# Optimization experiments

Hardware: AMD Instinct MI355X
Metric: run time of the kernel (lower is better)

The kernel has to match this reference:

```python
import jax, jax.numpy as jnp
import numpy as np
import math

D_MODEL, N_LEVELS, N_HEADS, N_POINTS = 256, 4, 8, 4
D_HEAD = D_MODEL // N_HEADS
SPATIAL = np.array([[128, 128], [64, 64], [32, 32], [16, 16]], dtype=np.int32)  # (H_l, W_l)
LEN_IN = int((SPATIAL[:, 0] * SPATIAL[:, 1]).sum())  # 21760
N_BATCH, LEN_Q = 8, 1000


def _offset_bias():
    # torch _reset_parameters grid_init
    thetas = np.arange(N_HEADS, dtype=np.float32) * (2.0 * math.pi / N_HEADS)
    grid = np.stack([np.cos(thetas), np.sin(thetas)], -1)
    grid = grid / np.abs(grid).max(-1, keepdims=True)
    grid = np.tile(grid.reshape(N_HEADS, 1, 1, 2), (1, N_LEVELS, N_POINTS, 1))
    for i in range(N_POINTS):
        grid[:, :, i, :] *= i + 1
    return jnp.asarray(grid.reshape(-1), dtype=jnp.float32)


def setup_inputs() -> dict:
    key = jax.random.key(0)
    ks = jax.random.split(key, 8)
    s = 1.0 / math.sqrt(D_MODEL)
    return {
        "query": jax.random.normal(ks[0], (N_BATCH, LEN_Q, D_MODEL), jnp.float32),
        "reference_points": jax.random.uniform(ks[1], (N_BATCH, LEN_Q, N_LEVELS, 2), jnp.float32),
        "input_flatten": jax.random.normal(ks[2], (N_BATCH, LEN_IN, D_MODEL), jnp.float32),
        "input_spatial_shapes": jnp.asarray(SPATIAL),
        "input_level_start_index": jnp.asarray(np.concatenate([[0], np.cumsum(SPATIAL[:, 0] * SPATIAL[:, 1])[:-1]]).astype(np.int32)),
        # params (W stored as (in, out); y = x @ W + b)
        "W_off": jax.random.normal(ks[3], (D_MODEL, N_HEADS * N_LEVELS * N_POINTS * 2), jnp.float32) * 0.01,
        "b_off": _offset_bias(),
        "W_attn": jax.random.normal(ks[4], (D_MODEL, N_HEADS * N_LEVELS * N_POINTS), jnp.float32) * 0.02,
        "b_attn": jnp.zeros((N_HEADS * N_LEVELS * N_POINTS,), jnp.float32),
        "W_val": jax.random.normal(ks[5], (D_MODEL, D_MODEL), jnp.float32) * s,
        "b_val": jnp.zeros((D_MODEL,), jnp.float32),
        "W_out": jax.random.normal(ks[6], (D_MODEL, D_MODEL), jnp.float32) * s,
        "b_out": jnp.zeros((D_MODEL,), jnp.float32),
    }


def _bilinear_sample(v, x, y, H, W):
    # v: (N, nH, H*W, dH); x, y: (N, nH, Lq, nP) in pixel coords (grid_sample align_corners=False, zeros padding)
    Nb, nH, Lq, nP = x.shape
    x0 = jnp.floor(x); y0 = jnp.floor(y)
    wx1 = x - x0; wy1 = y - y0
    x0i = x0.astype(jnp.int32); y0i = y0.astype(jnp.int32)
    out = jnp.zeros((Nb, nH, Lq, nP, v.shape[-1]), v.dtype)
    for dy, wy in ((0, 1.0 - wy1), (1, wy1)):
        for dx, wx in ((0, 1.0 - wx1), (1, wx1)):
            ix = x0i + dx; iy = y0i + dy
            valid = (ix >= 0) & (ix < W) & (iy >= 0) & (iy < H)
            idx = (jnp.clip(iy, 0, H - 1) * W + jnp.clip(ix, 0, W - 1)).reshape(Nb, nH, Lq * nP, 1)
            g = jnp.take_along_axis(v, idx, axis=2).reshape(Nb, nH, Lq, nP, -1)
            out = out + g * (wy * wx * valid.astype(v.dtype))[..., None]
    return out


def reference(query, reference_points, input_flatten, input_spatial_shapes, input_level_start_index,
              W_off, b_off, W_attn, b_attn, W_val, b_val, W_out, b_out):
    shapes = np.asarray(input_spatial_shapes)          # static metadata
    starts = np.asarray(input_level_start_index)
    Nb, Lq, _ = query.shape

    value = input_flatten @ W_val + b_val              # (N, Lin, C)
    value = value.reshape(Nb, -1, N_HEADS, D_HEAD).transpose(0, 2, 1, 3)  # (N, nH, Lin, dH)

    offsets = (query @ W_off + b_off).reshape(Nb, Lq, N_HEADS, N_LEVELS, N_POINTS, 2)
    attn = jax.nn.softmax((query @ W_attn + b_attn).reshape(Nb, Lq, N_HEADS, N_LEVELS * N_POINTS), axis=-1)
    attn = attn.reshape(Nb, Lq, N_HEADS, N_LEVELS, N_POINTS)

    # normalizer is (W_l, H_l) per level; locations in [0,1]
    normalizer = jnp.asarray(np.stack([shapes[:, 1], shapes[:, 0]], -1), jnp.float32)
    loc = reference_points[:, :, None, :, None, :] + offsets / normalizer[None, None, None, :, None, :]

    out = jnp.zeros((Nb, N_HEADS, Lq, D_HEAD), value.dtype)
    for l in range(N_LEVELS):
        H, W = int(shapes[l, 0]), int(shapes[l, 1])
        s = int(starts[l])
        v_l = value[:, :, s:s + H * W]                             # (N, nH, HW, dH)
        loc_l = loc[:, :, :, l].transpose(0, 2, 1, 3, 4)           # (N, nH, Lq, nP, 2)
        x = loc_l[..., 0] * W - 0.5
        y = loc_l[..., 1] * H - 0.5
        sampled = _bilinear_sample(v_l, x, y, H, W)                # (N, nH, Lq, nP, dH)
        a_l = attn[:, :, :, l].transpose(0, 2, 1, 3)               # (N, nH, Lq, nP)
        out = out + jnp.einsum('nhqpd,nhqp->nhqd', sampled, a_l)

    out = out.transpose(0, 2, 1, 3).reshape(Nb, Lq, D_MODEL)
    return out @ W_out + b_out
```

## Files before the change

kernel.cpp:

```cpp
#include <hip/hip_runtime.h>
#include <hip/hip_bf16.h>

#define D_MODEL 256
#define N_HEADS 8
#define D_HEAD 32
#define N_LEVELS 4
#define N_POINTS 4
#define LEN_IN 21760
#define N_BATCH 8
#define LEN_Q 1000

typedef __attribute__((ext_vector_type(8))) short short8;
typedef __attribute__((ext_vector_type(4))) float f32x4;
typedef __attribute__((ext_vector_type(4))) unsigned int u32x4;

typedef const __attribute__((address_space(1))) void* gp1;
typedef __attribute__((address_space(3))) void* lp3;

__device__ __forceinline__ unsigned short f2bf(float f) {
    unsigned int u = __float_as_uint(f);
    u += 0x7FFFu + ((u >> 16) & 1u);
    return (unsigned short)(u >> 16);
}
__device__ __forceinline__ float bf2f(unsigned short s) {
    return __uint_as_float(((unsigned int)s) << 16);
}

__global__ __launch_bounds__(256) void prep_kernel(
    const float* __restrict__ Wv, const float* __restrict__ Wo,
    const float* __restrict__ Wa, const float* __restrict__ Wu,
    const float* __restrict__ boff, const float* __restrict__ battn,
    unsigned short* __restrict__ WtVp, unsigned short* __restrict__ WtC,
    unsigned short* __restrict__ WtO, float* __restrict__ bcat)
{
    int idx = blockIdx.x * 256 + threadIdx.x;
    if (idx < 65536) {
        int j = idx & 7, lane = (idx >> 3) & 63, nf = (idx >> 9) & 15, ks = idx >> 13;
        int col = nf * 16 + (lane & 15);
        int k = ks * 32 + (lane >> 4) * 8 + j;
        WtVp[idx] = f2bf(Wv[k * 256 + col]);
    } else if (idx < 65536 + 98304) {
        int j = idx - 65536;
        int n = j >> 8, k = j & 255;
        float s = (n < 256) ? Wo[k * 256 + n] : Wa[k * 128 + (n - 256)];
        WtC[j] = f2bf(s);
    } else if (idx < 65536 + 98304 + 65536) {
        int j = idx - (65536 + 98304);
        int n = j >> 8, k = j & 255;
        WtO[j] = f2bf(Wu[k * 256 + n]);
    } else if (idx < 65536 + 98304 + 65536 + 384) {
        int j = idx - (65536 + 98304 + 65536);
        bcat[j] = (j < 256) ? boff[j] : battn[j - 256];
    }
}

__global__ __launch_bounds__(256) void gemm_value(
    const float* __restrict__ A,
    const unsigned short* __restrict__ Bp,
    const float* __restrict__ bias,
    unsigned short* __restrict__ C)
{
    __shared__ float lds[2][2048];

    const int tid = threadIdx.x;
    const int wave = tid >> 6, lane = tid & 63;
    const int lhi = lane >> 4, llo = lane & 15;
    const int mBase = blockIdx.x * 64;

    const int soff = tid * 16;
    const int r0 = soff >> 7, cb0 = soff & 127;
    const size_t g0 = (size_t)r0 * 1024 + (size_t)(cb0 ^ ((r0 & 7) << 4));
    const size_t g1 = g0 + (size_t)32 * 1024;

    const char* Ab = (const char*)(A + (size_t)mBase * 256);
    const int dsto = soff >> 2;

    f32x4 acc[4][4];
#pragma unroll
    for (int mf = 0; mf < 4; ++mf)
#pragma unroll
        for (int n = 0; n < 4; ++n)
            acc[mf][n] = (f32x4){0.f, 0.f, 0.f, 0.f};

    {
        float* dst0 = &lds[0][dsto];
        __builtin_amdgcn_global_load_lds((gp1)(const void*)(Ab + g0),
                                         (lp3)dst0, 16, 0, 0);
        __builtin_amdgcn_global_load_lds((gp1)(const void*)(Ab + g1),
                                         (lp3)(dst0 + 1024), 16, 0, 0);
    }

#pragma unroll
    for (int kt = 0; kt < 8; ++kt) {
        const int cur = kt & 1;

        short8 b[4];
#pragma unroll
        for (int n = 0; n < 4; ++n)
            b[n] = *reinterpret_cast<const short8*>(
                Bp + ((size_t)(kt * 16 + wave * 4 + n) * 64 + lane) * 8);

        if (kt < 7) {
            const size_t off = (size_t)(kt + 1) * 128;
            float* dst0 = &lds[cur ^ 1][dsto];
            __builtin_amdgcn_global_load_lds((gp1)(const void*)(Ab + off + g0),
                                             (lp3)dst0, 16, 0, 0);
            __builtin_amdgcn_global_load_lds((gp1)(const void*)(Ab + off + g1),
                                             (lp3)(dst0 + 1024), 16, 0, 0);
        }

        __builtin_amdgcn_sched_barrier(0);
        if (kt < 7) asm volatile("s_waitcnt vmcnt(2)" ::: "memory");
        else        asm volatile("s_waitcnt vmcnt(0)" ::: "memory");
        __builtin_amdgcn_sched_barrier(0);
        __builtin_amdgcn_s_barrier();
        __builtin_amdgcn_sched_barrier(0);

        short8 af[4];
#pragma unroll
        for (int mf = 0; mf < 4; ++mf) {
            const int row = mf * 16 + llo;
            const int sz = (llo & 7) << 4;
            const char* base = (const char*)&lds[cur][0] + row * 128;
            f32x4 flo = *reinterpret_cast<const f32x4*>(base + ((lhi * 32) ^ sz));
            f32x4 fhi = *reinterpret_cast<const f32x4*>(base + ((lhi * 32 + 16) ^ sz));
            short8 t;
            t[0] = (short)f2bf(flo[0]); t[1] = (short)f2bf(flo[1]);
            t[2] = (short)f2bf(flo[2]); t[3] = (short)f2bf(flo[3]);
            t[4] = (short)f2bf(fhi[0]); t[5] = (short)f2bf(fhi[1]);
            t[6] = (short)f2bf(fhi[2]); t[7] = (short)f2bf(fhi[3]);
            af[mf] = t;
        }

#pragma unroll
        for (int mf = 0; mf < 4; ++mf)
#pragma unroll
            for (int n = 0; n < 4; ++n)
                acc[mf][n] = __builtin_amdgcn_mfma_f32_16x16x32_bf16(
                    af[mf], b[n], acc[mf][n], 0, 0, 0);

        __builtin_amdgcn_sched_barrier(0);
        __builtin_amdgcn_s_barrier();
        __builtin_amdgcn_sched_barrier(0);
    }

#pragma unroll
    for (int mf = 0; mf < 4; ++mf) {
        const int row0 = mBase + mf * 16 + lhi * 4;
#pragma unroll
        for (int n = 0; n < 4; ++n) {
            const int col = wave * 64 + n * 16 + llo;
            const float bb = bias[col];
#pragma unroll
            for (int r = 0; r < 4; ++r)
                C[(size_t)(row0 + r) * 256 + col] = f2bf(acc[mf][n][r] + bb);
        }
    }
}

template<int NF, bool ABF16, bool OBF16>
__global__ __launch_bounds__(256) void gemm_k256(
    const void* __restrict__ Av, const unsigned short* __restrict__ Wt,
    const float* __restrict__ bias, void* __restrict__ Cv)
{
    const int wave = threadIdx.x >> 6;
    const int lane = threadIdx.x & 63;
    const int lhi = lane >> 4, llo = lane & 15;
    const int mBase = blockIdx.x * 16;
    const int colBase = wave * (NF * 16);
    const int N = NF * 64;

    f32x4 acc[NF];
#pragma unroll
    for (int n = 0; n < NF; ++n)
        acc[n] = (f32x4){0.f, 0.f, 0.f, 0.f};

#pragma unroll
    for (int ks = 0; ks < 8; ++ks) {
        const int kk = ks * 32 + lhi * 8;
        short8 a;
        if (ABF16) {
            a = *reinterpret_cast<const short8*>(
                (const unsigned short*)Av + (size_t)(mBase + llo) * 256 + kk);
        } else {
            const float* ap = (const float*)Av + (size_t)(mBase + llo) * 256 + kk;
            f32x4 f0 = *reinterpret_cast<const f32x4*>(ap);
            f32x4 f1 = *reinterpret_cast<const f32x4*>(ap + 4);
            short8 t;
            t[0] = (short)f2bf(f0[0]); t[1] = (short)f2bf(f0[1]);
            t[2] = (short)f2bf(f0[2]); t[3] = (short)f2bf(f0[3]);
            t[4] = (short)f2bf(f1[0]); t[5] = (short)f2bf(f1[1]);
            t[6] = (short)f2bf(f1[2]); t[7] = (short)f2bf(f1[3]);
            a = t;
        }
        short8 b[NF];
#pragma unroll
        for (int n = 0; n < NF; ++n) {
            const unsigned short* bp =
                Wt + (size_t)(colBase + n * 16 + llo) * 256 + kk;
            b[n] = *reinterpret_cast<const short8*>(bp);
        }
#pragma unroll
        for (int n = 0; n < NF; ++n)
            acc[n] = __builtin_amdgcn_mfma_f32_16x16x32_bf16(
                a, b[n], acc[n], 0, 0, 0);
    }

    const int row0 = mBase + lhi * 4;
#pragma unroll
    for (int n = 0; n < NF; ++n) {
        const int col = colBase + n * 16 + llo;
        const float bb = bias[col];
#pragma unroll
        for (int r = 0; r < 4; ++r) {
            float v = acc[n][r] + bb;
            size_t idx = (size_t)(row0 + r) * N + col;
            if (OBF16) ((unsigned short*)Cv)[idx] = f2bf(v);
            else       ((float*)Cv)[idx] = v;
        }
    }
}

__global__ __launch_bounds__(512) void ms_sample_kernel(
    const unsigned short* __restrict__ value,
    const float* __restrict__ proj,
    const float* __restrict__ refp,
    unsigned short* __restrict__ out_h)
{
    const int bid = blockIdx.x;
    const int b = bid & 7;
    const int q = bid >> 3;
    const int bq = b * LEN_Q + q;

    const int h = threadIdx.x >> 6;
    const int lane = threadIdx.x & 63;
    const int task = lane >> 2;
    const int l = task >> 2;
    const int qd = lane & 3;

    const float* prow = proj + (size_t)bq * 384;

    float lg = prow[256 + h * 16 + (lane & 15)];
    float mx = lg;
    mx = fmaxf(mx, __shfl_xor(mx, 1, 16));
    mx = fmaxf(mx, __shfl_xor(mx, 2, 16));
    mx = fmaxf(mx, __shfl_xor(mx, 4, 16));
    mx = fmaxf(mx, __shfl_xor(mx, 8, 16));
    float e = __expf(lg - mx);
    float den = e;
    den += __shfl_xor(den, 1, 16);
    den += __shfl_xor(den, 2, 16);
    den += __shfl_xor(den, 4, 16);
    den += __shfl_xor(den, 8, 16);
    const float wsm = e / den;
    const float ws = __shfl(wsm, task, 16);

    const int Wl = 128 >> l;
    const int st = (65536 - (65536 >> (l << 1))) / 3;

    const float dx = prow[h * 32 + 2 * task];
    const float dy = prow[h * 32 + 2 * task + 1];
    const float rx = refp[((size_t)bq * 4 + l) * 2 + 0];
    const float ry = refp[((size_t)bq * 4 + l) * 2 + 1];

    const float Wlf = (float)Wl;
    const float x = rx * Wlf + dx - 0.5f;
    const float y = ry * Wlf + dy - 0.5f;
    const float x0f = floorf(x), y0f = floorf(y);
    const int x0 = (int)x0f, y0 = (int)y0f;
    const float wx1 = x - x0f, wy1 = y - y0f;
    const float wx0 = 1.f - wx1, wy0 = 1.f - wy1;

    const int x0c = min(max(x0, 0), Wl - 1);
    const int x1c = min(max(x0 + 1, 0), Wl - 1);
    const int y0c = min(max(y0, 0), Wl - 1);
    const int y1c = min(max(y0 + 1, 0), Wl - 1);
    const float fx0 = (x0 >= 0 && x0 < Wl) ? 1.f : 0.f;
    const float fx1 = (x0 + 1 >= 0 && x0 + 1 < Wl) ? 1.f : 0.f;
    const float fy0 = (y0 >= 0 && y0 < Wl) ? 1.f : 0.f;
    const float fy1 = (y0 + 1 >= 0 && y0 + 1 < Wl) ? 1.f : 0.f;

    const int rr0 = st + y0c * Wl, rr1 = st + y1c * Wl;
    const int r00 = rr0 + x0c, r01 = rr0 + x1c;
    const int r10 = rr1 + x0c, r11 = rr1 + x1c;

    float wgt[4];
    wgt[0] = ws * wy0 * wx0 * fy0 * fx0;
    wgt[1] = ws * wy0 * wx1 * fy0 * fx1;
    wgt[2] = ws * wy1 * wx0 * fy1 * fx0;
    wgt[3] = ws * wy1 * wx1 * fy1 * fx1;

    const char* vb = (const char*)value + (size_t)b * LEN_IN * 512
                   + h * 64 + qd * 16;
    u32x4 v0 = *reinterpret_cast<const u32x4*>(vb + (size_t)r00 * 512);
    u32x4 v1 = *reinterpret_cast<const u32x4*>(vb + (size_t)r01 * 512);
    u32x4 v2 = *reinterpret_cast<const u32x4*>(vb + (size_t)r10 * 512);
    u32x4 v3 = *reinterpret_cast<const u32x4*>(vb + (size_t)r11 * 512);

    float acc[8];
#pragma unroll
    for (int j = 0; j < 8; ++j) acc[j] = 0.f;
#pragma unroll
    for (int n = 0; n < 4; ++n) {
        const u32x4 v = (n == 0) ? v0 : (n == 1) ? v1 : (n == 2) ? v2 : v3;
        const float wn = wgt[n];
#pragma unroll
        for (int j = 0; j < 4; ++j) {
            const unsigned int u = v[j];
            acc[2 * j]     += wn * bf2f((unsigned short)(u & 0xFFFFu));
            acc[2 * j + 1] += wn * bf2f((unsigned short)(u >> 16));
        }
    }

#pragma unroll
    for (int j = 0; j < 8; ++j) {
        acc[j] += __shfl_xor(acc[j], 4, 64);
        acc[j] += __shfl_xor(acc[j], 8, 64);
        acc[j] += __shfl_xor(acc[j], 16, 64);
        acc[j] += __shfl_xor(acc[j], 32, 64);
    }

    if (task == 0) {
        u32x4 o;
#pragma unroll
        for (int j = 0; j < 4; ++j)
            o[j] = (unsigned int)f2bf(acc[2 * j]) |
                   ((unsigned int)f2bf(acc[2 * j + 1]) << 16);
        *reinterpret_cast<u32x4*>(
            out_h + (size_t)bq * 256 + h * 32 + qd * 8) = o;
    }
}

extern "C" void kernel_launch(void* const* d_in, const int* in_sizes, int n_in,
                              void* d_out, int out_size, void* d_ws, size_t ws_size,
                              hipStream_t stream)
{
    const float* query  = (const float*)d_in[0];
    const float* refp   = (const float*)d_in[1];
    const float* inpf   = (const float*)d_in[2];
    const float* W_off  = (const float*)d_in[5];
    const float* b_off  = (const float*)d_in[6];
    const float* W_attn = (const float*)d_in[7];
    const float* b_attn = (const float*)d_in[8];
    const float* W_val  = (const float*)d_in[9];
    const float* b_val  = (const float*)d_in[10];
    const float* W_out  = (const float*)d_in[11];
    const float* b_out  = (const float*)d_in[12];

    char* ws = (char*)d_ws;
    unsigned short* value = (unsigned short*)(ws);
    float*          proj  = (float*)(ws + 89128960);
    unsigned short* out_h = (unsigned short*)(ws + 89128960 + 12288000);
    unsigned short* WtVp  = (unsigned short*)(ws + 109608960);
    unsigned short* WtC   = (unsigned short*)(ws + 109740032);
    unsigned short* WtO   = (unsigned short*)(ws + 109936640);
    float*          bcat  = (float*)(ws + 110067712);

    prep_kernel<<<898, 256, 0, stream>>>(W_val, W_off, W_attn, W_out,
                                         b_off, b_attn, WtVp, WtC, WtO, bcat);

    gemm_value<<<(N_BATCH * LEN_IN) / 64, 256, 0, stream>>>(
        inpf, WtVp, b_val, value);

    gemm_k256<6, false, false><<<(N_BATCH * LEN_Q) / 16, 256, 0, stream>>>(
        query, WtC, bcat, (void*)proj);

    ms_sample_kernel<<<N_BATCH * LEN_Q, 512, 0, stream>>>(
        value, proj, refp, out_h);

    gemm_k256<4, true, false><<<(N_BATCH * LEN_Q) / 16, 256, 0, stream>>>(
        out_h, WtO, b_out, d_out);
}
```

Before: 132.2 us.

## Merge value and query projection GEMMs into one launch; hoist sampling loads

The value-projection GEMM and the query offset/attention projection GEMM now run in a single heterogeneous launch. The first 500 blocks compute the query projection and the remaining 2720 compute the value projection, which removes one kernel launch and lets the small GEMM share the GPU with the large one instead of running serially. Separately, the sampling kernel now issues its offset, reference-point and value gathers before the softmax reductions, using float2 loads, so memory latency overlaps with the shuffle math. The proj blocks still declare the large LDS array, which may lower occupancy for those blocks.

```diff
diff --git a/kernel.cpp b/kernel.cpp
--- a/kernel.cpp
+++ b/kernel.cpp
@@ -9,6 +9,9 @@
 #define LEN_IN 21760
 #define N_BATCH 8
 #define LEN_Q 1000
+
+#define PROJ_BLOCKS 500
+#define VAL_BLOCKS 2720
 
 typedef __attribute__((ext_vector_type(8))) short short8;
 typedef __attribute__((ext_vector_type(4))) float f32x4;
@@ -54,18 +57,66 @@
     }
 }
 
-__global__ __launch_bounds__(256) void gemm_value(
+__global__ __launch_bounds__(256) void fused_vp_kernel(
     const float* __restrict__ A,
     const unsigned short* __restrict__ Bp,
-    const float* __restrict__ bias,
-    unsigned short* __restrict__ C)
+    const float* __restrict__ biasV,
+    unsigned short* __restrict__ C,
+    const float* __restrict__ Q,
+    const unsigned short* __restrict__ WtC,
+    const float* __restrict__ bcat,
+    float* __restrict__ proj)
 {
     __shared__ float lds[2][2048];
 
     const int tid = threadIdx.x;
     const int wave = tid >> 6, lane = tid & 63;
     const int lhi = lane >> 4, llo = lane & 15;
-    const int mBase = blockIdx.x * 64;
+
+    if (blockIdx.x < PROJ_BLOCKS) {
+        const int mBase = blockIdx.x * 16;
+        const int colBase = wave * 96;
+
+        f32x4 acc[6];
+#pragma unroll
+        for (int n = 0; n < 6; ++n)
+            acc[n] = (f32x4){0.f, 0.f, 0.f, 0.f};
+
+#pragma unroll
+        for (int ks = 0; ks < 8; ++ks) {
+            const int kk = ks * 32 + lhi * 8;
+            const float* ap = Q + (size_t)(mBase + llo) * 256 + kk;
+            f32x4 f0 = *reinterpret_cast<const f32x4*>(ap);
+            f32x4 f1 = *reinterpret_cast<const f32x4*>(ap + 4);
+            short8 a;
+            a[0] = (short)f2bf(f0[0]); a[1] = (short)f2bf(f0[1]);
+            a[2] = (short)f2bf(f0[2]); a[3] = (short)f2bf(f0[3]);
+            a[4] = (short)f2bf(f1[0]); a[5] = (short)f2bf(f1[1]);
+            a[6] = (short)f2bf(f1[2]); a[7] = (short)f2bf(f1[3]);
+            short8 b[6];
+#pragma unroll
+            for (int n = 0; n < 6; ++n)
+                b[n] = *reinterpret_cast<const short8*>(
+                    WtC + (size_t)(colBase + n * 16 + llo) * 256 + kk);
+#pragma unroll
+            for (int n = 0; n < 6; ++n)
+                acc[n] = __builtin_amdgcn_mfma_f32_16x16x32_bf16(
+                    a, b[n], acc[n], 0, 0, 0);
+        }
+
+        const int row0 = mBase + lhi * 4;
+#pragma unroll
+        for (int n = 0; n < 6; ++n) {
+            const int col = colBase + n * 16 + llo;
+            const float bb = bcat[col];
+#pragma unroll
+            for (int r = 0; r < 4; ++r)
+                proj[(size_t)(row0 + r) * 384 + col] = acc[n][r] + bb;
+        }
+        return;
+    }
+
+    const int mBase = (blockIdx.x - PROJ_BLOCKS) * 64;
 
     const int soff = tid * 16;
     const int r0 = soff >> 7, cb0 = soff & 127;
@@ -150,7 +201,7 @@
 #pragma unroll
         for (int n = 0; n < 4; ++n) {
             const int col = wave * 64 + n * 16 + llo;
-            const float bb = bias[col];
+            const float bb = biasV[col];
 #pragma unroll
             for (int r = 0; r < 4; ++r)
                 C[(size_t)(row0 + r) * 256 + col] = f2bf(acc[mf][n][r] + bb);
@@ -240,6 +291,40 @@
 
     const float* prow = proj + (size_t)bq * 384;
 
+    const int Wl = 128 >> l;
+    const int st = (65536 - (65536 >> (l << 1))) / 3;
+
+    const float2 dxy = *reinterpret_cast<const float2*>(prow + h * 32 + 2 * task);
+    const float2 rxy = *reinterpret_cast<const float2*>(refp + ((size_t)bq * 4 + l) * 2);
+
+    const float Wlf = (float)Wl;
+    const float x = rxy.x * Wlf + dxy.x - 0.5f;
+    const float y = rxy.y * Wlf + dxy.y - 0.5f;
+    const float x0f = floorf(x), y0f = floorf(y);
+    const int x0 = (int)x0f, y0 = (int)y0f;
+    const float wx1 = x - x0f, wy1 = y - y0f;
+    const float wx0 = 1.f - wx1, wy0 = 1.f - wy1;
+
+    const int x0c = min(max(x0, 0), Wl - 1);
+    const int x1c = min(max(x0 + 1, 0), Wl - 1);
+    const int y0c = min(max(y0, 0), Wl - 1);
+    const int y1c = min(max(y0 + 1, 0), Wl - 1);
+    const float fx0 = (x0 >= 0 && x0 < Wl) ? 1.f : 0.f;
+    const float fx1 = (x0 + 1 >= 0 && x0 + 1 < Wl) ? 1.f : 0.f;
+    const float fy0 = (y0 >= 0 && y0 < Wl) ? 1.f : 0.f;
+    const float fy1 = (y0 + 1 >= 0 && y0 + 1 < Wl) ? 1.f : 0.f;
+
+    const int rr0 = st + y0c * Wl, rr1 = st + y1c * Wl;
+    const int r00 = rr0 + x0c, r01 = rr0 + x1c;
+    const int r10 = rr1 + x0c, r11 = rr1 + x1c;
+
+    const char* vb = (const char*)value + (size_t)b * LEN_IN * 512
+                   + h * 64 + qd * 16;
+    u32x4 v0 = *reinterpret_cast<const u32x4*>(vb + (size_t)r00 * 512);
+    u32x4 v1 = *reinterpret_cast<const u32x4*>(vb + (size_t)r01 * 512);
+    u32x4 v2 = *reinterpret_cast<const u32x4*>(vb + (size_t)r10 * 512);
+    u32x4 v3 = *reinterpret_cast<const u32x4*>(vb + (size_t)r11 * 512);
+
     float lg = prow[256 + h * 16 + (lane & 15)];
     float mx = lg;
     mx = fmaxf(mx, __shfl_xor(mx, 1, 16));
@@ -255,47 +340,11 @@
     const float wsm = e / den;
     const float ws = __shfl(wsm, task, 16);
 
-    const int Wl = 128 >> l;
-    const int st = (65536 - (65536 >> (l << 1))) / 3;
-
-    const float dx = prow[h * 32 + 2 * task];
-    const float dy = prow[h * 32 + 2 * task + 1];
-    const float rx = refp[((size_t)bq * 4 + l) * 2 + 0];
-    const float ry = refp[((size_t)bq * 4 + l) * 2 + 1];
-
-    const float Wlf = (float)Wl;
-    const float x = rx * Wlf + dx - 0.5f;
-    const float y = ry * Wlf + dy - 0.5f;
-    const float x0f = floorf(x), y0f = floorf(y);
-    const int x0 = (int)x0f, y0 = (int)y0f;
-    const float wx1 = x - x0f, wy1 = y - y0f;
-    const float wx0 = 1.f - wx1, wy0 = 1.f - wy1;
-
-    const int x0c = min(max(x0, 0), Wl - 1);
-    const int x1c = min(max(x0 + 1, 0), Wl - 1);
-    const int y0c = min(max(y0, 0), Wl - 1);
-    const int y1c = min(max(y0 + 1, 0), Wl - 1);
-    const float fx0 = (x0 >= 0 && x0 < Wl) ? 1.f : 0.f;
-    const float fx1 = (x0 + 1 >= 0 && x0 + 1 < Wl) ? 1.f : 0.f;
-    const float fy0 = (y0 >= 0 && y0 < Wl) ? 1.f : 0.f;
-    const float fy1 = (y0 + 1 >= 0 && y0 + 1 < Wl) ? 1.f : 0.f;
-
-    const int rr0 = st + y0c * Wl, rr1 = st + y1c * Wl;
-    const int r00 = rr0 + x0c, r01 = rr0 + x1c;
-    const int r10 = rr1 + x0c, r11 = rr1 + x1c;
-
     float wgt[4];
     wgt[0] = ws * wy0 * wx0 * fy0 * fx0;
     wgt[1] = ws * wy0 * wx1 * fy0 * fx1;
     wgt[2] = ws * wy1 * wx0 * fy1 * fx0;
     wgt[3] = ws * wy1 * wx1 * fy1 * fx1;
-
-    const char* vb = (const char*)value + (size_t)b * LEN_IN * 512
-                   + h * 64 + qd * 16;
-    u32x4 v0 = *reinterpret_cast<const u32x4*>(vb + (size_t)r00 * 512);
-    u32x4 v1 = *reinterpret_cast<const u32x4*>(vb + (size_t)r01 * 512);
-    u32x4 v2 = *reinterpret_cast<const u32x4*>(vb + (size_t)r10 * 512);
-    u32x4 v3 = *reinterpret_cast<const u32x4*>(vb + (size_t)r11 * 512);
 
     float acc[8];
 #pragma unroll
@@ -359,11 +408,8 @@
     prep_kernel<<<898, 256, 0, stream>>>(W_val, W_off, W_attn, W_out,
                                          b_off, b_attn, WtVp, WtC, WtO, bcat);
 
-    gemm_value<<<(N_BATCH * LEN_IN) / 64, 256, 0, stream>>>(
-        inpf, WtVp, b_val, value);
-
-    gemm_k256<6, false, false><<<(N_BATCH * LEN_Q) / 16, 256, 0, stream>>>(
-        query, WtC, bcat, (void*)proj);
+    fused_vp_kernel<<<PROJ_BLOCKS + VAL_BLOCKS, 256, 0, stream>>>(
+        inpf, WtVp, b_val, value, query, WtC, bcat, proj);
 
     ms_sample_kernel<<<N_BATCH * LEN_Q, 512, 0, stream>>>(
         value, proj, refp, out_h);
```

New measurement: 139.7 us. 5.7% more time.

## Triple-buffer value GEMM A tiles, prefetch B fragments, hoist sampling gathers

Applied to the files above, without the earlier changes.

The value-projection GEMM moves from a double to a triple LDS buffer, staging two K-tiles ahead, and register-prefetches the next B fragments one iteration early so global latency overlaps the MFMA work. The sampling kernel now issues the four bilinear value gathers before the softmax shuffle reduction, and loads offsets and reference points as float2, so the gather latency hides behind the softmax arithmetic. This costs more LDS per block, which may lower occupancy, and more live registers in both kernels. The hand-set vmcnt counts must match the number of outstanding loads exactly.

```diff
diff --git a/kernel.cpp b/kernel.cpp
--- a/kernel.cpp
+++ b/kernel.cpp
@@ -60,7 +60,7 @@
     const float* __restrict__ bias,
     unsigned short* __restrict__ C)
 {
-    __shared__ float lds[2][2048];
+    __shared__ float lds[3][2048];
 
     const int tid = threadIdx.x;
     const int wave = tid >> 6, lane = tid & 63;
@@ -71,10 +71,17 @@
     const int r0 = soff >> 7, cb0 = soff & 127;
     const size_t g0 = (size_t)r0 * 1024 + (size_t)(cb0 ^ ((r0 & 7) << 4));
     const size_t g1 = g0 + (size_t)32 * 1024;
-
     const char* Ab = (const char*)(A + (size_t)mBase * 256);
     const int dsto = soff >> 2;
 
+#define STAGE(t) { \
+        float* dst0 = &lds[(t) % 3][dsto]; \
+        const size_t off_ = (size_t)(t) * 128; \
+        __builtin_amdgcn_global_load_lds((gp1)(const void*)(Ab + off_ + g0), \
+                                         (lp3)dst0, 16, 0, 0); \
+        __builtin_amdgcn_global_load_lds((gp1)(const void*)(Ab + off_ + g1), \
+                                         (lp3)(dst0 + 1024), 16, 0, 0); }
+
     f32x4 acc[4][4];
 #pragma unroll
     for (int mf = 0; mf < 4; ++mf)
@@ -82,36 +89,29 @@
         for (int n = 0; n < 4; ++n)
             acc[mf][n] = (f32x4){0.f, 0.f, 0.f, 0.f};
 
-    {
-        float* dst0 = &lds[0][dsto];
-        __builtin_amdgcn_global_load_lds((gp1)(const void*)(Ab + g0),
-                                         (lp3)dst0, 16, 0, 0);
-        __builtin_amdgcn_global_load_lds((gp1)(const void*)(Ab + g1),
-                                         (lp3)(dst0 + 1024), 16, 0, 0);
-    }
+    short8 bcur[4], bnxt[4];
+
+#pragma unroll
+    for (int n = 0; n < 4; ++n)
+        bcur[n] = *reinterpret_cast<const short8*>(
+            Bp + ((size_t)(0 * 16 + wave * 4 + n) * 64 + lane) * 8);
+    STAGE(0);
+    STAGE(1);
 
 #pragma unroll
     for (int kt = 0; kt < 8; ++kt) {
-        const int cur = kt & 1;
-
-        short8 b[4];
-#pragma unroll
-        for (int n = 0; n < 4; ++n)
-            b[n] = *reinterpret_cast<const short8*>(
-                Bp + ((size_t)(kt * 16 + wave * 4 + n) * 64 + lane) * 8);
-
         if (kt < 7) {
-            const size_t off = (size_t)(kt + 1) * 128;
-            float* dst0 = &lds[cur ^ 1][dsto];
-            __builtin_amdgcn_global_load_lds((gp1)(const void*)(Ab + off + g0),
-                                             (lp3)dst0, 16, 0, 0);
-            __builtin_amdgcn_global_load_lds((gp1)(const void*)(Ab + off + g1),
-                                             (lp3)(dst0 + 1024), 16, 0, 0);
-        }
-
-        __builtin_amdgcn_sched_barrier(0);
-        if (kt < 7) asm volatile("s_waitcnt vmcnt(2)" ::: "memory");
-        else        asm volatile("s_waitcnt vmcnt(0)" ::: "memory");
+#pragma unroll
+            for (int n = 0; n < 4; ++n)
+                bnxt[n] = *reinterpret_cast<const short8*>(
+                    Bp + ((size_t)((kt + 1) * 16 + wave * 4 + n) * 64 + lane) * 8);
+        }
+        if (kt < 6) STAGE(kt + 2);
+
+        __builtin_amdgcn_sched_barrier(0);
+        if (kt < 6)      asm volatile("s_waitcnt vmcnt(8)" ::: "memory");
+        else if (kt == 6) asm volatile("s_waitcnt vmcnt(6)" ::: "memory");
+        else              asm volatile("s_waitcnt vmcnt(0)" ::: "memory");
         __builtin_amdgcn_sched_barrier(0);
         __builtin_amdgcn_s_barrier();
         __builtin_amdgcn_sched_barrier(0);
@@ -121,7 +121,7 @@
         for (int mf = 0; mf < 4; ++mf) {
             const int row = mf * 16 + llo;
             const int sz = (llo & 7) << 4;
-            const char* base = (const char*)&lds[cur][0] + row * 128;
+            const char* base = (const char*)&lds[kt % 3][0] + row * 128;
             f32x4 flo = *reinterpret_cast<const f32x4*>(base + ((lhi * 32) ^ sz));
             f32x4 fhi = *reinterpret_cast<const f32x4*>(base + ((lhi * 32 + 16) ^ sz));
             short8 t;
@@ -137,12 +137,18 @@
 #pragma unroll
             for (int n = 0; n < 4; ++n)
                 acc[mf][n] = __builtin_amdgcn_mfma_f32_16x16x32_bf16(
-                    af[mf], b[n], acc[mf][n], 0, 0, 0);
+                    af[mf], bcur[n], acc[mf][n], 0, 0, 0);
+
+        if (kt < 7) {
+#pragma unroll
+            for (int n = 0; n < 4; ++n) bcur[n] = bnxt[n];
+        }
 
         __builtin_amdgcn_sched_barrier(0);
         __builtin_amdgcn_s_barrier();
         __builtin_amdgcn_sched_barrier(0);
     }
+#undef STAGE
 
 #pragma unroll
     for (int mf = 0; mf < 4; ++mf) {
@@ -240,6 +246,40 @@
 
     const float* prow = proj + (size_t)bq * 384;
 
+    const int Wl = 128 >> l;
+    const int st = (65536 - (65536 >> (l << 1))) / 3;
+
+    const float2 dxy = *reinterpret_cast<const float2*>(prow + h * 32 + 2 * task);
+    const float2 rxy = *reinterpret_cast<const float2*>(refp + ((size_t)bq * 4 + l) * 2);
+
+    const float Wlf = (float)Wl;
+    const float x = rxy.x * Wlf + dxy.x - 0.5f;
+    const float y = rxy.y * Wlf + dxy.y - 0.5f;
+    const float x0f = floorf(x), y0f = floorf(y);
+    const int x0 = (int)x0f, y0 = (int)y0f;
+    const float wx1 = x - x0f, wy1 = y - y0f;
+    const float wx0 = 1.f - wx1, wy0 = 1.f - wy1;
+
+    const int x0c = min(max(x0, 0), Wl - 1);
+    const int x1c = min(max(x0 + 1, 0), Wl - 1);
+    const int y0c = min(max(y0, 0), Wl - 1);
+    const int y1c = min(max(y0 + 1, 0), Wl - 1);
+    const float fx0 = (x0 >= 0 && x0 < Wl) ? 1.f : 0.f;
+    const float fx1 = (x0 + 1 >= 0 && x0 + 1 < Wl) ? 1.f : 0.f;
+    const float fy0 = (y0 >= 0 && y0 < Wl) ? 1.f : 0.f;
+    const float fy1 = (y0 + 1 >= 0 && y0 + 1 < Wl) ? 1.f : 0.f;
+
+    const int rr0 = st + y0c * Wl, rr1 = st + y1c * Wl;
+    const int r00 = rr0 + x0c, r01 = rr0 + x1c;
+    const int r10 = rr1 + x0c, r11 = rr1 + x1c;
+
+    const char* vb = (const char*)value + (size_t)b * LEN_IN * 512
+                   + h * 64 + qd * 16;
+    u32x4 v0 = *reinterpret_cast<const u32x4*>(vb + (size_t)r00 * 512);
+    u32x4 v1 = *reinterpret_cast<const u32x4*>(vb + (size_t)r01 * 512);
+    u32x4 v2 = *reinterpret_cast<const u32x4*>(vb + (size_t)r10 * 512);
+    u32x4 v3 = *reinterpret_cast<const u32x4*>(vb + (size_t)r11 * 512);
+
     float lg = prow[256 + h * 16 + (lane & 15)];
     float mx = lg;
     mx = fmaxf(mx, __shfl_xor(mx, 1, 16));
@@ -255,47 +295,11 @@
     const float wsm = e / den;
     const float ws = __shfl(wsm, task, 16);
 
-    const int Wl = 128 >> l;
-    const int st = (65536 - (65536 >> (l << 1))) / 3;
-
-    const float dx = prow[h * 32 + 2 * task];
-    const float dy = prow[h * 32 + 2 * task + 1];
-    const float rx = refp[((size_t)bq * 4 + l) * 2 + 0];
-    const float ry = refp[((size_t)bq * 4 + l) * 2 + 1];
-
-    const float Wlf = (float)Wl;
-    const float x = rx * Wlf + dx - 0.5f;
-    const float y = ry * Wlf + dy - 0.5f;
-    const float x0f = floorf(x), y0f = floorf(y);
-    const int x0 = (int)x0f, y0 = (int)y0f;
-    const float wx1 = x - x0f, wy1 = y - y0f;
-    const float wx0 = 1.f - wx1, wy0 = 1.f - wy1;
-
-    const int x0c = min(max(x0, 0), Wl - 1);
-    const int x1c = min(max(x0 + 1, 0), Wl - 1);
-    const int y0c = min(max(y0, 0), Wl - 1);
-    const int y1c = min(max(y0 + 1, 0), Wl - 1);
-    const float fx0 = (x0 >= 0 && x0 < Wl) ? 1.f : 0.f;
-    const float fx1 = (x0 + 1 >= 0 && x0 + 1 < Wl) ? 1.f : 0.f;
-    const float fy0 = (y0 >= 0 && y0 < Wl) ? 1.f : 0.f;
-    const float fy1 = (y0 + 1 >= 0 && y0 + 1 < Wl) ? 1.f : 0.f;
-
-    const int rr0 = st + y0c * Wl, rr1 = st + y1c * Wl;
-    const int r00 = rr0 + x0c, r01 = rr0 + x1c;
-    const int r10 = rr1 + x0c, r11 = rr1 + x1c;
-
     float wgt[4];
     wgt[0] = ws * wy0 * wx0 * fy0 * fx0;
     wgt[1] = ws * wy0 * wx1 * fy0 * fx1;
     wgt[2] = ws * wy1 * wx0 * fy1 * fx0;
     wgt[3] = ws * wy1 * wx1 * fy1 * fx1;
-
-    const char* vb = (const char*)value + (size_t)b * LEN_IN * 512
-                   + h * 64 + qd * 16;
-    u32x4 v0 = *reinterpret_cast<const u32x4*>(vb + (size_t)r00 * 512);
-    u32x4 v1 = *reinterpret_cast<const u32x4*>(vb + (size_t)r01 * 512);
-    u32x4 v2 = *reinterpret_cast<const u32x4*>(vb + (size_t)r10 * 512);
-    u32x4 v3 = *reinterpret_cast<const u32x4*>(vb + (size_t)r11 * 512);
 
     float acc[8];
 #pragma unroll
```

Measured after the change: 137.2 us. 3.8% more time.
